# Kernel tuning notes

Measured on AMD Instinct MI355X. Metric: run time of the kernel, lower is better.

## Reference

```python
import jax, jax.numpy as jnp
import numpy as np

N_NODES = 100000
N_EDGES = 3200000
N_FEAT = 128
HIDDEN = 64
N_CLASSES = 3
N_GRAPHS = 512
BN_EPS = 1e-5


def setup_inputs() -> dict:
    key = jax.random.key(0)
    ks = jax.random.split(key, 16)
    x = jax.random.normal(ks[0], (N_NODES, N_FEAT), dtype=jnp.float32)
    edge_index = jax.random.randint(ks[1], (2, N_EDGES), 0, N_NODES, dtype=jnp.int64)
    batch = jnp.sort(jax.random.randint(ks[2], (N_NODES,), 0, N_GRAPHS, dtype=jnp.int64))
    # GCNConv weights (glorot-ish scale), biases
    W1 = jax.random.normal(ks[3], (N_FEAT, HIDDEN), dtype=jnp.float32) / np.sqrt(N_FEAT)
    b1 = jnp.zeros((HIDDEN,), dtype=jnp.float32)
    W2 = jax.random.normal(ks[4], (HIDDEN, HIDDEN), dtype=jnp.float32) / np.sqrt(HIDDEN)
    b2 = jnp.zeros((HIDDEN,), dtype=jnp.float32)
    # BatchNorm params + running stats (eval mode)
    g1 = jnp.ones((HIDDEN,), dtype=jnp.float32)
    bt1 = jnp.zeros((HIDDEN,), dtype=jnp.float32)
    rm1 = jax.random.normal(ks[5], (HIDDEN,), dtype=jnp.float32) * 0.1
    rv1 = jax.random.uniform(ks[6], (HIDDEN,), dtype=jnp.float32) + 0.5
    g2 = jnp.ones((HIDDEN,), dtype=jnp.float32)
    bt2 = jnp.zeros((HIDDEN,), dtype=jnp.float32)
    rm2 = jax.random.normal(ks[7], (HIDDEN,), dtype=jnp.float32) * 0.1
    rv2 = jax.random.uniform(ks[8], (HIDDEN,), dtype=jnp.float32) + 0.5
    # classifier
    Wc = jax.random.normal(ks[9], (HIDDEN, N_CLASSES), dtype=jnp.float32) / np.sqrt(HIDDEN)
    bc = jnp.zeros((N_CLASSES,), dtype=jnp.float32)
    return dict(x=x, W1=W1, b1=b1, g1=g1, bt1=bt1, rm1=rm1, rv1=rv1,
                W2=W2, b2=b2, g2=g2, bt2=bt2, rm2=rm2, rv2=rv2,
                Wc=Wc, bc=bc, edge_index=edge_index, batch=batch)


def _gcn_conv(x, W, b, src, dst):
    # x' = D^{-1/2} (A + I) D^{-1/2} X W + b  (PyG GCNConv with self-loops)
    n = x.shape[0]
    h = x @ W  # [N, H]
    loops = jnp.arange(n, dtype=src.dtype)
    s = jnp.concatenate([src, loops])
    d = jnp.concatenate([dst, loops])
    deg = jax.ops.segment_sum(jnp.ones_like(d, dtype=h.dtype), d, num_segments=n)
    dinv = jnp.where(deg > 0, jax.lax.rsqrt(deg), 0.0)
    norm = dinv[s] * dinv[d]  # [E+N]
    msg = h[s] * norm[:, None]  # gather + scale
    out = jax.ops.segment_sum(msg, d, num_segments=n)  # scatter-add
    return out + b


def _bn_eval(x, gamma, beta, rmean, rvar):
    return (x - rmean) * jax.lax.rsqrt(rvar + BN_EPS) * gamma + beta


def reference(x, W1, b1, g1, bt1, rm1, rv1, W2, b2, g2, bt2, rm2, rv2, Wc, bc, edge_index, batch):
    src, dst = edge_index[0], edge_index[1]
    h = _gcn_conv(x, W1, b1, src, dst)
    h = jax.nn.relu(_bn_eval(h, g1, bt1, rm1, rv1))
    # dropout inactive in eval mode
    h = _gcn_conv(h, W2, b2, src, dst)
    h = jax.nn.relu(_bn_eval(h, g2, bt2, rm2, rv2))
    # global mean pool over graphs
    sums = jax.ops.segment_sum(h, batch, num_segments=N_GRAPHS)
    cnts = jax.ops.segment_sum(jnp.ones((h.shape[0],), dtype=h.dtype), batch, num_segments=N_GRAPHS)
    pooled = sums / jnp.maximum(cnts, 1.0)[:, None]  # [G, H]
    return pooled @ Wc + bc  # [G, C]
```

## Files before the change

### kernel.cpp

```cpp
#include <hip/hip_runtime.h>

#define NN 100000
#define NE 3200000
#define NG 512
#define NCB 782
#define BN_EPS 1e-5f

typedef unsigned short u16;
typedef unsigned int u32;

__device__ __forceinline__ u16 f2bf(float f) {
    u32 u = __float_as_uint(f);
    u += 0x7FFF + ((u >> 16) & 1);
    return (u16)(u >> 16);
}

__global__ __launch_bounds__(256) void k_chist(const int* __restrict__ dst, int* __restrict__ ccount) {
    __shared__ int h[NCB];
    int t = threadIdx.x;
    for (int i = t; i < NCB; i += 256) h[i] = 0;
    __syncthreads();
    int stride = gridDim.x * 256;
    for (int e = blockIdx.x * 256 + t; e < NE; e += stride)
        atomicAdd(&h[dst[e] >> 7], 1);
    __syncthreads();
    for (int i = t; i < NCB; i += 256)
        if (h[i]) atomicAdd(&ccount[i], h[i]);
}

__global__ __launch_bounds__(256) void k_cscan(const int* __restrict__ ccount, int* __restrict__ cbase,
                                               int* __restrict__ fbase, int* __restrict__ gcur) {
    __shared__ int sh[256], sh2[256];
    int t = threadIdx.x;
    int v[4], w[4];
    int s = 0, s2 = 0;
#pragma unroll
    for (int j = 0; j < 4; j++) {
        int idx = t * 4 + j;
        int c = (idx < NCB) ? ccount[idx] : 0;
        v[j] = c;
        w[j] = (idx < NCB) ? ((c + 387) & ~3) : 0;
        s += v[j]; s2 += w[j];
    }
    sh[t] = s; sh2[t] = s2;
    __syncthreads();
    for (int off = 1; off < 256; off <<= 1) {
        int x = (t >= off) ? sh[t - off] : 0;
        int x2 = (t >= off) ? sh2[t - off] : 0;
        __syncthreads();
        sh[t] += x; sh2[t] += x2;
        __syncthreads();
    }
    int run = sh[t] - s, run2 = sh2[t] - s2;
#pragma unroll
    for (int j = 0; j < 4; j++) {
        int idx = t * 4 + j;
        if (idx < NCB) { cbase[idx] = run; gcur[idx] = run; fbase[idx] = run2; }
        run += v[j]; run2 += w[j];
    }
    if (t == 255) cbase[NCB] = run;
}

#define P1_CHUNK 16384
__global__ __launch_bounds__(1024) void k_p1(const int* __restrict__ src, const int* __restrict__ dst,
                                             int* __restrict__ gcur, int* __restrict__ esc) {
    __shared__ int ccur[NCB];
    const int t = threadIdx.x;
    const int e0 = blockIdx.x * P1_CHUNK;
    for (int i = t; i < NCB; i += 1024) ccur[i] = 0;
    __syncthreads();
    int n = NE - e0; if (n > P1_CHUNK) n = P1_CHUNK;
    for (int idx = t; idx < n; idx += 1024)
        atomicAdd(&ccur[dst[e0 + idx] >> 7], 1);
    __syncthreads();
    for (int i = t; i < NCB; i += 1024) {
        int c = ccur[i];
        ccur[i] = (c > 0) ? atomicAdd(&gcur[i], c) : 0;
    }
    __syncthreads();
    for (int idx = t; idx < n; idx += 1024) {
        int dd = dst[e0 + idx];
        int s = src[e0 + idx];
        int pos = atomicAdd(&ccur[dd >> 7], 1);
        esc[pos] = s | ((dd & 127) << 17);
    }
}

__global__ __launch_bounds__(256) void k_p2(const int* __restrict__ esc, const int* __restrict__ cbase,
                                            const int* __restrict__ fbase, int* __restrict__ esf,
                                            int* __restrict__ offs, int* __restrict__ cntp,
                                            float* __restrict__ dinv) {
    __shared__ int lcnt[128], loff[128], lcur[128];
    int t = threadIdx.x, b = blockIdx.x;
    int c0 = cbase[b], c1 = cbase[b + 1];
    if (t < 128) lcnt[t] = 0;
    __syncthreads();
    for (int i = c0 + t; i < c1; i += 256) atomicAdd(&lcnt[esc[i] >> 17], 1);
    __syncthreads();
    int p = 0, cnt = 0;
    if (t < 128) { cnt = lcnt[t]; p = (cnt + 3) & ~3; loff[t] = p; }
    __syncthreads();
    for (int off = 1; off < 128; off <<= 1) {
        int x = (t >= off && t < 128) ? loff[t - off] : 0;
        __syncthreads();
        if (t < 128) loff[t] += x;
        __syncthreads();
    }
    int fb = fbase[b];
    int node = (b << 7) + t;
    if (t < 128) {
        int o = fb + loff[t] - p;
        lcur[t] = o;
        if (node < NN) {
            offs[node] = o;
            cntp[node] = p;
            dinv[node] = rsqrtf((float)(cnt + 1));
            for (int q = cnt; q < p; q++) esf[o + q] = NN;
        }
    }
    __syncthreads();
    for (int i = c0 + t; i < c1; i += 256) {
        int rec = esc[i];
        int pos = atomicAdd(&lcur[rec >> 17], 1);
        esf[pos] = rec & 0x1FFFF;
    }
}

template <int K>
__global__ __launch_bounds__(256) void k_gemm(const float* __restrict__ X,
                                              const float* __restrict__ W,
                                              const float* __restrict__ dinv,
                                              u16* __restrict__ hp, int M) {
    __shared__ float xs[128 * 68];
    __shared__ float ws[64 * 64];
    const int t = threadIdx.x;
    const int row0 = blockIdx.x * 128;
    const int rg = t >> 3;
    const int f0 = (t & 7) * 8;

    float acc[4][8];
#pragma unroll
    for (int j = 0; j < 4; j++)
#pragma unroll
        for (int c = 0; c < 8; c++) acc[j][c] = 0.0f;

    for (int kc = 0; kc < K; kc += 64) {
        __syncthreads();
        const float4* Wg = (const float4*)(W + (size_t)kc * 64);
        float4* ws4 = (float4*)ws;
#pragma unroll
        for (int i = 0; i < 4; i++) ws4[t + i * 256] = Wg[t + i * 256];
#pragma unroll
        for (int p = 0; p < 8; p++) {
            int rr = p * 16 + (t >> 4);
            int c4 = (t & 15) * 4;
            int row = row0 + rr;
            float4 v = make_float4(0.f, 0.f, 0.f, 0.f);
            if (row < M) v = *(const float4*)(X + (size_t)row * K + kc + c4);
            *(float4*)(&xs[rr * 68 + c4]) = v;
        }
        __syncthreads();

        for (int kk = 0; kk < 64; kk += 4) {
            float4 xv[4];
#pragma unroll
            for (int j = 0; j < 4; j++)
                xv[j] = *(const float4*)(&xs[(rg + 32 * j) * 68 + kk]);
#pragma unroll
            for (int kki = 0; kki < 4; kki++) {
                float4 w0 = *(const float4*)(&ws[(kk + kki) * 64 + f0]);
                float4 w1 = *(const float4*)(&ws[(kk + kki) * 64 + f0 + 4]);
#pragma unroll
                for (int j = 0; j < 4; j++) {
                    float a = (&xv[j].x)[kki];
                    acc[j][0] = fmaf(a, w0.x, acc[j][0]);
                    acc[j][1] = fmaf(a, w0.y, acc[j][1]);
                    acc[j][2] = fmaf(a, w0.z, acc[j][2]);
                    acc[j][3] = fmaf(a, w0.w, acc[j][3]);
                    acc[j][4] = fmaf(a, w1.x, acc[j][4]);
                    acc[j][5] = fmaf(a, w1.y, acc[j][5]);
                    acc[j][6] = fmaf(a, w1.z, acc[j][6]);
                    acc[j][7] = fmaf(a, w1.w, acc[j][7]);
                }
            }
        }
    }

#pragma unroll
    for (int j = 0; j < 4; j++) {
        int row = row0 + rg + 32 * j;
        if (row < M) {
            float di = dinv[row];
            uint4 pk;
            pk.x = (u32)f2bf(acc[j][0] * di) | ((u32)f2bf(acc[j][1] * di) << 16);
            pk.y = (u32)f2bf(acc[j][2] * di) | ((u32)f2bf(acc[j][3] * di) << 16);
            pk.z = (u32)f2bf(acc[j][4] * di) | ((u32)f2bf(acc[j][5] * di) << 16);
            pk.w = (u32)f2bf(acc[j][6] * di) | ((u32)f2bf(acc[j][7] * di) << 16);
            *(uint4*)(hp + (size_t)row * 64 + f0) = pk;
        }
    }
}

__global__ __launch_bounds__(256) void k_agg(const u32* __restrict__ hp2,
                                             const int* __restrict__ esf,
                                             const int* __restrict__ offs,
                                             const int* __restrict__ cntp,
                                             const float* __restrict__ dinv,
                                             const float* __restrict__ bias,
                                             const float* __restrict__ gam,
                                             const float* __restrict__ bet,
                                             const float* __restrict__ rm,
                                             const float* __restrict__ rv,
                                             float* __restrict__ out) {
    const int lane = threadIdx.x & 63;
    const int half = lane >> 5;
    const int fp = lane & 31;
    const int node = (blockIdx.x * 256 + threadIdx.x) >> 6;
    if (node >= NN) return;
    const int beg = offs[node];
    const int mp = cntp[node];
    float ax = 0.0f, ay = 0.0f;
    for (int c = 0; c < mp; c += 64) {
        int m = mp - c;
        if (m > 64) m = 64;
        int rec = (lane < m) ? esf[beg + c + lane] : NN;
        int j = 0;
        for (; j + 16 <= m; j += 16) {
            u32 v[8];
#pragma unroll
            for (int u = 0; u < 8; u++) {
                int s = __shfl(rec, j + 2 * u + half);
                v[u] = hp2[(size_t)s * 32 + fp];
            }
#pragma unroll
            for (int u = 0; u < 8; u++) {
                ax += __uint_as_float(v[u] << 16);
                ay += __uint_as_float(v[u] & 0xFFFF0000u);
            }
        }
        for (; j < m; j += 4) {
            int s0 = __shfl(rec, j + half);
            int s1 = __shfl(rec, j + 2 + half);
            u32 v0 = hp2[(size_t)s0 * 32 + fp];
            u32 v1 = hp2[(size_t)s1 * 32 + fp];
            ax += __uint_as_float(v0 << 16);
            ay += __uint_as_float(v0 & 0xFFFF0000u);
            ax += __uint_as_float(v1 << 16);
            ay += __uint_as_float(v1 & 0xFFFF0000u);
        }
    }
    ax += __shfl_xor(ax, 32);
    ay += __shfl_xor(ay, 32);
    u32 sv = hp2[(size_t)node * 32 + fp];
    ax += __uint_as_float(sv << 16);
    ay += __uint_as_float(sv & 0xFFFF0000u);

    const float di = dinv[node];
    const int f0 = fp * 2;
    float2 bia = *(const float2*)(bias + f0);
    float2 ga  = *(const float2*)(gam + f0);
    float2 be  = *(const float2*)(bet + f0);
    float2 rme = *(const float2*)(rm + f0);
    float2 rva = *(const float2*)(rv + f0);
    float vx = ax * di + bia.x;
    float vy = ay * di + bia.y;
    float yx = (vx - rme.x) * (ga.x * rsqrtf(rva.x + BN_EPS)) + be.x;
    float yy = (vy - rme.y) * (ga.y * rsqrtf(rva.y + BN_EPS)) + be.y;
    if (half == 0)
        *(float2*)(out + (size_t)node * 64 + f0) = make_float2(fmaxf(yx, 0.0f), fmaxf(yy, 0.0f));
}

__global__ __launch_bounds__(256) void k_poolcls(const float* __restrict__ h,
                                                 const int* __restrict__ batch,
                                                 const float* __restrict__ Wc,
                                                 const float* __restrict__ bc,
                                                 float* __restrict__ out) {
    __shared__ float sh[256];
    const int g = blockIdx.x;
    const int t = threadIdx.x;
    const int lane = t & 63;
    const int wv = t >> 6;
    int lo = 0, hi = NN;
    while (lo < hi) { int mid = (lo + hi) >> 1; if (batch[mid] < g) lo = mid + 1; else hi = mid; }
    const int r0 = lo;
    hi = NN;
    while (lo < hi) { int mid = (lo + hi) >> 1; if (batch[mid] < g + 1) lo = mid + 1; else hi = mid; }
    const int r1 = lo;
    float acc = 0.0f;
    for (int r = r0 + wv; r < r1; r += 4)
        acc += h[(size_t)r * 64 + lane];
    sh[t] = acc;
    __syncthreads();
    if (wv == 0) {
        float p = sh[lane] + sh[64 + lane] + sh[128 + lane] + sh[192 + lane];
        p *= 1.0f / fmaxf((float)(r1 - r0), 1.0f);
        float c0 = p * Wc[lane * 3 + 0];
        float c1 = p * Wc[lane * 3 + 1];
        float c2 = p * Wc[lane * 3 + 2];
        for (int o = 32; o > 0; o >>= 1) {
            c0 += __shfl_xor(c0, o);
            c1 += __shfl_xor(c1, o);
            c2 += __shfl_xor(c2, o);
        }
        if (lane == 0) {
            out[g * 3 + 0] = c0 + bc[0];
            out[g * 3 + 1] = c1 + bc[1];
            out[g * 3 + 2] = c2 + bc[2];
        }
    }
}

extern "C" void kernel_launch(void* const* d_in, const int* in_sizes, int n_in,
                              void* d_out, int out_size, void* d_ws, size_t ws_size,
                              hipStream_t stream) {
    const float* x   = (const float*)d_in[0];
    const float* W1  = (const float*)d_in[1];
    const float* b1  = (const float*)d_in[2];
    const float* g1  = (const float*)d_in[3];
    const float* bt1 = (const float*)d_in[4];
    const float* rm1 = (const float*)d_in[5];
    const float* rv1 = (const float*)d_in[6];
    const float* W2  = (const float*)d_in[7];
    const float* b2  = (const float*)d_in[8];
    const float* g2  = (const float*)d_in[9];
    const float* bt2 = (const float*)d_in[10];
    const float* rm2 = (const float*)d_in[11];
    const float* rv2 = (const float*)d_in[12];
    const float* Wc  = (const float*)d_in[13];
    const float* bc  = (const float*)d_in[14];
    const int* ei    = (const int*)d_in[15];
    const int* batch = (const int*)d_in[16];
    const int* srcp = ei;
    const int* dstp = ei + NE;

    char* ws = (char*)d_ws;
    u16*   hpb    = (u16*)(ws);
    int*   ccount = (int*)(ws + 12800128);
    int*   cbase  = (int*)(ws + 12803264);
    int*   fbase  = (int*)(ws + 12806400);
    int*   gcur   = (int*)(ws + 12809536);
    int*   offs   = (int*)(ws + 12812672);
    int*   cntp   = (int*)(ws + 13212672);
    float* dinv   = (float*)(ws + 13612672);
    int*   esf    = (int*)(ws + 14012672);
    float* bufB   = (float*)(ws + 28052672);
    int*   esc    = (int*)(ws + 28052672);

    hipMemsetAsync(hpb + (size_t)NN * 64, 0, 128 + NCB * 4, stream);

    k_chist<<<512, 256, 0, stream>>>(dstp, ccount);
    k_cscan<<<1, 256, 0, stream>>>(ccount, cbase, fbase, gcur);
    k_p1<<<(NE + P1_CHUNK - 1) / P1_CHUNK, 1024, 0, stream>>>(srcp, dstp, gcur, esc);
    k_p2<<<NCB, 256, 0, stream>>>(esc, cbase, fbase, esf, offs, cntp, dinv);

    k_gemm<128><<<(NN + 127) / 128, 256, 0, stream>>>(x, W1, dinv, hpb, NN);
    k_agg<<<(NN * 64 + 255) / 256, 256, 0, stream>>>((const u32*)hpb, esf, offs, cntp, dinv, b1, g1, bt1, rm1, rv1, bufB);

    k_gemm<64><<<(NN + 127) / 128, 256, 0, stream>>>(bufB, W2, dinv, hpb, NN);
    k_agg<<<(NN * 64 + 255) / 256, 256, 0, stream>>>((const u32*)hpb, esf, offs, cntp, dinv, b2, g2, bt2, rm2, rv2, bufB);

    k_poolcls<<<NG, 256, 0, stream>>>(bufB, batch, Wc, bc, (float*)d_out);
}
```

Before: 394.5 us.

## Split bf16 feature table into four column slices for aggregation locality

The GEMM output is stored as four 16-feature slices, each a contiguous [NN+1][16] bf16 array, and aggregation runs one grid pass per slice. Each wave handles 8 edges at once with 8 lanes per edge, so each gathered row is 32 bytes. The intent is that a slice table (about 3.2 MB) fits in cache better than the full 12.8 MB table, improving gather hit rates. The cost is reading the edge list four times, plus a cross-lane reduction and more blocks. The zero padding row is now written in the scan kernel rather than by a memset.

New measurement: 569.0 us. +44.2%, slower.

```diff
diff --git a/kernel.cpp b/kernel.cpp
--- a/kernel.cpp
+++ b/kernel.cpp
@@ -5,6 +5,9 @@
 #define NG 512
 #define NCB 782
 #define BN_EPS 1e-5f
+#define NSLICE 4
+#define SLICE_U32 8
+#define BPS 25000
 
 typedef unsigned short u16;
 typedef unsigned int u32;
@@ -29,9 +32,14 @@
 }
 
 __global__ __launch_bounds__(256) void k_cscan(const int* __restrict__ ccount, int* __restrict__ cbase,
-                                               int* __restrict__ fbase, int* __restrict__ gcur) {
+                                               int* __restrict__ fbase, int* __restrict__ gcur,
+                                               u32* __restrict__ hpz) {
     __shared__ int sh[256], sh2[256];
     int t = threadIdx.x;
+    if (t < NSLICE * SLICE_U32) {
+        int slice = t >> 3, w = t & 7;
+        hpz[(size_t)slice * (NN + 1) * SLICE_U32 + (size_t)NN * SLICE_U32 + w] = 0;
+    }
     int v[4], w[4];
     int s = 0, s2 = 0;
 #pragma unroll
@@ -186,6 +194,8 @@
         }
     }
 
+    const int slice = f0 >> 4;
+    const int rem = f0 & 15;
 #pragma unroll
     for (int j = 0; j < 4; j++) {
         int row = row0 + rg + 32 * j;
@@ -196,12 +206,16 @@
             pk.y = (u32)f2bf(acc[j][2] * di) | ((u32)f2bf(acc[j][3] * di) << 16);
             pk.z = (u32)f2bf(acc[j][4] * di) | ((u32)f2bf(acc[j][5] * di) << 16);
             pk.w = (u32)f2bf(acc[j][6] * di) | ((u32)f2bf(acc[j][7] * di) << 16);
-            *(uint4*)(hp + (size_t)row * 64 + f0) = pk;
-        }
-    }
-}
-
-__global__ __launch_bounds__(256) void k_agg(const u32* __restrict__ hp2,
+            *(uint4*)(hp + ((size_t)slice * (NN + 1) + row) * 16 + rem) = pk;
+        }
+    }
+}
+
+#define ACC1(vv) do { \
+    alo += __uint_as_float((vv) << 16); \
+    ahi += __uint_as_float((vv) & 0xFFFF0000u); } while (0)
+
+__global__ __launch_bounds__(256) void k_agg(const u32* __restrict__ hp,
                                              const int* __restrict__ esf,
                                              const int* __restrict__ offs,
                                              const int* __restrict__ cntp,
@@ -212,62 +226,59 @@
                                              const float* __restrict__ rm,
                                              const float* __restrict__ rv,
                                              float* __restrict__ out) {
+    const int slice = blockIdx.x / BPS;
+    const int node = (blockIdx.x % BPS) * 4 + (threadIdx.x >> 6);
     const int lane = threadIdx.x & 63;
-    const int half = lane >> 5;
-    const int fp = lane & 31;
-    const int node = (blockIdx.x * 256 + threadIdx.x) >> 6;
-    if (node >= NN) return;
+    const int g8 = lane >> 3;
+    const int fp = lane & 7;
+    const u32* hs = hp + (size_t)slice * (NN + 1) * SLICE_U32;
+
     const int beg = offs[node];
     const int mp = cntp[node];
-    float ax = 0.0f, ay = 0.0f;
+
+    float alo = 0.0f, ahi = 0.0f;
+    if (g8 == 0) { u32 sv = hs[node * SLICE_U32 + fp]; ACC1(sv); }
+
     for (int c = 0; c < mp; c += 64) {
-        int m = mp - c;
-        if (m > 64) m = 64;
+        int m = mp - c; if (m > 64) m = 64;
         int rec = (lane < m) ? esf[beg + c + lane] : NN;
-        int j = 0;
-        for (; j + 16 <= m; j += 16) {
-            u32 v[8];
-#pragma unroll
-            for (int u = 0; u < 8; u++) {
-                int s = __shfl(rec, j + 2 * u + half);
-                v[u] = hp2[(size_t)s * 32 + fp];
-            }
-#pragma unroll
-            for (int u = 0; u < 8; u++) {
-                ax += __uint_as_float(v[u] << 16);
-                ay += __uint_as_float(v[u] & 0xFFFF0000u);
-            }
-        }
-        for (; j < m; j += 4) {
-            int s0 = __shfl(rec, j + half);
-            int s1 = __shfl(rec, j + 2 + half);
-            u32 v0 = hp2[(size_t)s0 * 32 + fp];
-            u32 v1 = hp2[(size_t)s1 * 32 + fp];
-            ax += __uint_as_float(v0 << 16);
-            ay += __uint_as_float(v0 & 0xFFFF0000u);
-            ax += __uint_as_float(v1 << 16);
-            ay += __uint_as_float(v1 & 0xFFFF0000u);
-        }
-    }
-    ax += __shfl_xor(ax, 32);
-    ay += __shfl_xor(ay, 32);
-    u32 sv = hp2[(size_t)node * 32 + fp];
-    ax += __uint_as_float(sv << 16);
-    ay += __uint_as_float(sv & 0xFFFF0000u);
-
-    const float di = dinv[node];
-    const int f0 = fp * 2;
-    float2 bia = *(const float2*)(bias + f0);
-    float2 ga  = *(const float2*)(gam + f0);
-    float2 be  = *(const float2*)(bet + f0);
-    float2 rme = *(const float2*)(rm + f0);
-    float2 rva = *(const float2*)(rv + f0);
-    float vx = ax * di + bia.x;
-    float vy = ay * di + bia.y;
-    float yx = (vx - rme.x) * (ga.x * rsqrtf(rva.x + BN_EPS)) + be.x;
-    float yy = (vy - rme.y) * (ga.y * rsqrtf(rva.y + BN_EPS)) + be.y;
-    if (half == 0)
+        int s;
+        s = __shfl(rec, g8);      u32 v0 = hs[s * SLICE_U32 + fp];
+        s = __shfl(rec, 8 + g8);  u32 v1 = hs[s * SLICE_U32 + fp];
+        s = __shfl(rec, 16 + g8); u32 v2 = hs[s * SLICE_U32 + fp];
+        s = __shfl(rec, 24 + g8); u32 v3 = hs[s * SLICE_U32 + fp];
+        const bool h4 = (m > 32);
+        u32 v4 = 0, v5 = 0, v6 = 0, v7 = 0;
+        if (h4) {
+            s = __shfl(rec, 32 + g8); v4 = hs[s * SLICE_U32 + fp];
+            s = __shfl(rec, 40 + g8); v5 = hs[s * SLICE_U32 + fp];
+            s = __shfl(rec, 48 + g8); v6 = hs[s * SLICE_U32 + fp];
+            s = __shfl(rec, 56 + g8); v7 = hs[s * SLICE_U32 + fp];
+        }
+        ACC1(v0); ACC1(v1); ACC1(v2); ACC1(v3);
+        if (h4) { ACC1(v4); ACC1(v5); ACC1(v6); ACC1(v7); }
+    }
+
+#pragma unroll
+    for (int off = 8; off <= 32; off <<= 1) {
+        alo += __shfl_xor(alo, off);
+        ahi += __shfl_xor(ahi, off);
+    }
+
+    if (g8 == 0) {
+        const float di = dinv[node];
+        const int f0 = slice * 16 + fp * 2;
+        float2 bi = *(const float2*)(bias + f0);
+        float2 ga = *(const float2*)(gam + f0);
+        float2 be = *(const float2*)(bet + f0);
+        float2 rme = *(const float2*)(rm + f0);
+        float2 rva = *(const float2*)(rv + f0);
+        float vx = alo * di + bi.x;
+        float vy = ahi * di + bi.y;
+        float yx = (vx - rme.x) * (ga.x * rsqrtf(rva.x + BN_EPS)) + be.x;
+        float yy = (vy - rme.y) * (ga.y * rsqrtf(rva.y + BN_EPS)) + be.y;
         *(float2*)(out + (size_t)node * 64 + f0) = make_float2(fmaxf(yx, 0.0f), fmaxf(yy, 0.0f));
+    }
 }
 
 __global__ __launch_bounds__(256) void k_poolcls(const float* __restrict__ h,
@@ -346,18 +357,18 @@
     float* bufB   = (float*)(ws + 28052672);
     int*   esc    = (int*)(ws + 28052672);
 
-    hipMemsetAsync(hpb + (size_t)NN * 64, 0, 128 + NCB * 4, stream);
+    hipMemsetAsync(ccount, 0, NCB * 4, stream);
 
     k_chist<<<512, 256, 0, stream>>>(dstp, ccount);
-    k_cscan<<<1, 256, 0, stream>>>(ccount, cbase, fbase, gcur);
+    k_cscan<<<1, 256, 0, stream>>>(ccount, cbase, fbase, gcur, (u32*)hpb);
     k_p1<<<(NE + P1_CHUNK - 1) / P1_CHUNK, 1024, 0, stream>>>(srcp, dstp, gcur, esc);
     k_p2<<<NCB, 256, 0, stream>>>(esc, cbase, fbase, esf, offs, cntp, dinv);
 
     k_gemm<128><<<(NN + 127) / 128, 256, 0, stream>>>(x, W1, dinv, hpb, NN);
-    k_agg<<<(NN * 64 + 255) / 256, 256, 0, stream>>>((const u32*)hpb, esf, offs, cntp, dinv, b1, g1, bt1, rm1, rv1, bufB);
+    k_agg<<<NSLICE * BPS, 256, 0, stream>>>((const u32*)hpb, esf, offs, cntp, dinv, b1, g1, bt1, rm1, rv1, bufB);
 
     k_gemm<64><<<(NN + 127) / 128, 256, 0, stream>>>(bufB, W2, dinv, hpb, NN);
-    k_agg<<<(NN * 64 + 255) / 256, 256, 0, stream>>>((const u32*)hpb, esf, offs, cntp, dinv, b2, g2, bt2, rm2, rv2, bufB);
+    k_agg<<<NSLICE * BPS, 256, 0, stream>>>((const u32*)hpb, esf, offs, cntp, dinv, b2, g2, bt2, rm2, rv2, bufB);
 
     k_poolcls<<<NG, 256, 0, stream>>>(bufB, batch, Wc, bc, (float*)d_out);
 }
```
